# Kernel tuning notes

Hardware: AMD Instinct MI355X
Metric: run time of the kernel (lower is better)

Reference implementation:

```python
import jax, jax.numpy as jnp
import numpy as np

ALPHA = 1000.0


def setup_inputs() -> dict:
    key = jax.random.key(0)
    ks = jax.random.split(key, 5)
    B, D_in, K = 8192, 2048, 256  # K = n_clusters = embed_dim (square cluster_reps)
    x = jax.random.normal(ks[0], (B, D_in), dtype=jnp.float32)
    W_enc = jax.random.normal(ks[1], (D_in, K), dtype=jnp.float32) * (1.0 / np.sqrt(D_in))
    b_enc = jnp.zeros((K,), dtype=jnp.float32)
    W_dec = jax.random.normal(ks[2], (K, D_in), dtype=jnp.float32) * (1.0 / np.sqrt(K))
    b_dec = jnp.zeros((D_in,), dtype=jnp.float32)
    cluster_reps = jax.random.normal(ks[3], (K, K), dtype=jnp.float32)
    return {"x": x, "W_enc": W_enc, "b_enc": b_enc, "W_dec": W_dec,
            "b_dec": b_dec, "cluster_reps": cluster_reps}


def reference(x, W_enc, b_enc, W_dec, b_dec, cluster_reps):
    # Autoencoder (linear MLP stand-in for the injected module)
    emb = x @ W_enc + b_enc                    # [B, K]
    reconstruction = emb @ W_dec + b_dec       # [B, D_in]

    # Squared Euclidean distance to each cluster rep, in GEMM form: [B, K]
    # dist[b, k] = ||emb_b||^2 - 2 emb_b . c_k + ||c_k||^2
    dist = (jnp.sum(emb * emb, axis=1, keepdims=True)
            - 2.0 * (emb @ cluster_reps.T)
            + jnp.sum(cluster_reps * cluster_reps, axis=1)[None, :])

    stack_dist = dist.T                        # [K, B] (matches torch.stack over clusters)
    min_dist = jnp.min(stack_dist, axis=0)     # [B]
    stack_exp = jnp.exp(-ALPHA * (stack_dist - min_dist[None, :]))  # stable softmin
    softmax = stack_exp / jnp.sum(stack_exp, axis=0, keepdims=True)
    weighted_dist = stack_dist * softmax       # [K, B]
    return weighted_dist, reconstruction
```

## Files before the change

kernel.cpp:

```cpp
#include <hip/hip_runtime.h>

#define ALPHA_F 1000.0f

typedef _Float16 half8 __attribute__((ext_vector_type(8)));
typedef float floatx4 __attribute__((ext_vector_type(4)));

__device__ __forceinline__ void gload_lds16(const void* g, void* l) {
    __builtin_amdgcn_global_load_lds(
        (const __attribute__((address_space(1))) unsigned int*)g,
        (__attribute__((address_space(3))) unsigned int*)l, 16, 0, 0);
}

__global__ __launch_bounds__(256) void split_wenc(
    const float* __restrict__ W, _Float16* __restrict__ Wh, _Float16* __restrict__ Wl)
{
    const int q = blockIdx.x * 256 + threadIdx.x;
    const int n = q & 255, k8 = q >> 8;
    const int k = k8 * 8;
    half8 h, l;
    #pragma unroll
    for (int i = 0; i < 8; ++i) {
        const float v = W[(size_t)(k + i) * 256 + n] * 256.0f;
        const _Float16 hi = (_Float16)v;
        h[i] = hi;
        l[i] = (_Float16)(v - (float)hi);
    }
    const int kc = k >> 5, nt = n >> 4;
    const int lane = (n & 15) | ((k8 & 3) << 4);
    const size_t idx = (size_t)((kc * 16 + nt) * 64 + lane) * 8;
    *(half8*)(Wh + idx) = h;
    *(half8*)(Wl + idx) = l;
}

__global__ __launch_bounds__(256) void split_wdec(
    const float* __restrict__ W, _Float16* __restrict__ Wh)
{
    const int q = blockIdx.x * 256 + threadIdx.x;
    const int n = q & 2047, k8 = q >> 11;
    const int k = k8 * 8;
    half8 h;
    #pragma unroll
    for (int i = 0; i < 8; ++i) h[i] = (_Float16)W[(size_t)(k + i) * 2048 + n];
    const int kc = k8 >> 2, nt = n >> 4;
    const int lane = (n & 15) | ((k8 & 3) << 4);
    *(half8*)(Wh + (size_t)((kc * 128 + nt) * 64 + lane) * 8) = h;
}

__global__ __launch_bounds__(256) void split_creps(
    const float* __restrict__ C, _Float16* __restrict__ Ch, _Float16* __restrict__ Cl)
{
    const int q = blockIdx.x * 256 + threadIdx.x;
    const int n = q & 255, j8 = q >> 8;
    const int j = j8 * 8;
    half8 h, l;
    #pragma unroll
    for (int i = 0; i < 8; ++i) {
        const float v = C[(size_t)n * 256 + j + i];
        const _Float16 hi = (_Float16)v;
        h[i] = hi;
        l[i] = (_Float16)((v - (float)hi) * 2048.0f);
    }
    const int jc = j >> 5, nt = n >> 4;
    const int lane = (n & 15) | ((j8 & 3) << 4);
    const size_t idx = (size_t)((jc * 16 + nt) * 64 + lane) * 8;
    *(half8*)(Ch + idx) = h;
    *(half8*)(Cl + idx) = l;
}

__global__ __launch_bounds__(256) void emb_gemm(
    const float* __restrict__ x, const _Float16* __restrict__ Wh,
    const _Float16* __restrict__ Wl, float* __restrict__ P)
{
    __shared__ _Float16 Ah[4 * 64 * 8], Al[4 * 64 * 8];
    __shared__ _Float16 Bh[16 * 64 * 8], Bl[16 * 64 * 8];
    const int t = threadIdx.x, lane = t & 63, w = t >> 6;
    const int kk = blockIdx.x;
    const int mb = blockIdx.y;
    const int m0 = mb * 64;

    const int am = t >> 2, q = t & 3;
    _Float16* AhW = Ah + (((am >> 4) * 64) + ((am & 15) | (q << 4))) * 8;
    _Float16* AlW = Al + (((am >> 4) * 64) + ((am & 15) | (q << 4))) * 8;
    const float* xP = x + (size_t)(m0 + am) * 2048 + kk * 512 + q * 8;

    floatx4 acc[4][4] = {};

    for (int it = 0; it < 16; ++it) {
        const float4 v0 = *(const float4*)(xP + it * 32);
        const float4 v1 = *(const float4*)(xP + it * 32 + 4);
        const int kc = kk * 16 + it;
        __syncthreads();
        const _Float16* bh_src = Wh + (size_t)kc * 16 * 512;
        const _Float16* bl_src = Wl + (size_t)kc * 16 * 512;
        #pragma unroll
        for (int i = 0; i < 4; ++i) {
            const int c = w * 4 + i;
            gload_lds16(bh_src + (size_t)c * 512 + lane * 8, Bh + c * 512);
            gload_lds16(bl_src + (size_t)c * 512 + lane * 8, Bl + c * 512);
        }
        half8 h8, l8;
        {
            const float vv[8] = {v0.x, v0.y, v0.z, v0.w, v1.x, v1.y, v1.z, v1.w};
            #pragma unroll
            for (int i = 0; i < 8; ++i) {
                const _Float16 hi = (_Float16)vv[i];
                h8[i] = hi;
                l8[i] = (_Float16)(vv[i] - (float)hi);
            }
        }
        *(half8*)AhW = h8;
        *(half8*)AlW = l8;
        __syncthreads();

        half8 ah[4], al[4], bh[4], bl[4];
        #pragma unroll
        for (int s = 0; s < 4; ++s) {
            ah[s] = *(const half8*)(Ah + (s * 64 + lane) * 8);
            al[s] = *(const half8*)(Al + (s * 64 + lane) * 8);
        }
        #pragma unroll
        for (int ni = 0; ni < 4; ++ni) {
            bh[ni] = *(const half8*)(Bh + ((w * 4 + ni) * 64 + lane) * 8);
            bl[ni] = *(const half8*)(Bl + ((w * 4 + ni) * 64 + lane) * 8);
        }
        #pragma unroll
        for (int mi = 0; mi < 4; ++mi) {
            #pragma unroll
            for (int ni = 0; ni < 4; ++ni) {
                acc[mi][ni] = __builtin_amdgcn_mfma_f32_16x16x32_f16(ah[mi], bl[ni], acc[mi][ni], 0, 0, 0);
                acc[mi][ni] = __builtin_amdgcn_mfma_f32_16x16x32_f16(al[mi], bh[ni], acc[mi][ni], 0, 0, 0);
                acc[mi][ni] = __builtin_amdgcn_mfma_f32_16x16x32_f16(ah[mi], bh[ni], acc[mi][ni], 0, 0, 0);
            }
        }
    }

    float* Pk = P + (size_t)kk * 2097152;
    #pragma unroll
    for (int mi = 0; mi < 4; ++mi) {
        #pragma unroll
        for (int ni = 0; ni < 4; ++ni) {
            const int col = w * 64 + ni * 16 + (lane & 15);
            const int rowBase = m0 + mi * 16 + (lane >> 4) * 4;
            #pragma unroll
            for (int r = 0; r < 4; ++r)
                Pk[(size_t)(rowBase + r) * 256 + col] = acc[mi][ni][r];
        }
    }
}

__global__ __launch_bounds__(256) void finalize(
    const float* __restrict__ P, const float* __restrict__ b_enc,
    _Float16* __restrict__ eh, _Float16* __restrict__ el,
    float* __restrict__ enorm)
{
    const int t = threadIdx.x;
    const int row = blockIdx.x * 8 + (t >> 5);
    const int q = t & 31;
    const float* p = P + (size_t)row * 256 + q * 8;

    float4 s0 = *(const float4*)(p);
    float4 s1 = *(const float4*)(p + 4);
    #pragma unroll
    for (int kk = 1; kk < 4; ++kk) {
        const float4 a0 = *(const float4*)(p + (size_t)kk * 2097152);
        const float4 a1 = *(const float4*)(p + (size_t)kk * 2097152 + 4);
        s0.x += a0.x; s0.y += a0.y; s0.z += a0.z; s0.w += a0.w;
        s1.x += a1.x; s1.y += a1.y; s1.z += a1.z; s1.w += a1.w;
    }
    const float4 b0 = *(const float4*)(b_enc + q * 8);
    const float4 b1 = *(const float4*)(b_enc + q * 8 + 4);
    const float inv = 1.0f / 256.0f;
    float v[8];
    v[0] = s0.x * inv + b0.x; v[1] = s0.y * inv + b0.y;
    v[2] = s0.z * inv + b0.z; v[3] = s0.w * inv + b0.w;
    v[4] = s1.x * inv + b1.x; v[5] = s1.y * inv + b1.y;
    v[6] = s1.z * inv + b1.z; v[7] = s1.w * inv + b1.w;

    half8 h, l;
    float ssq = 0.0f;
    #pragma unroll
    for (int i = 0; i < 8; ++i) {
        const _Float16 hi = (_Float16)v[i];
        h[i] = hi;
        l[i] = (_Float16)((v[i] - (float)hi) * 2048.0f);
        ssq += v[i] * v[i];
    }
    const size_t idx = (size_t)(((row >> 4) * 8 + (q >> 2)) * 64
                                + ((row & 15) | ((q & 3) << 4))) * 8;
    *(half8*)(eh + idx) = h;
    *(half8*)(el + idx) = l;

    #pragma unroll
    for (int off = 16; off >= 1; off >>= 1) ssq += __shfl_xor(ssq, off, 64);
    if ((t & 31) == 0) enorm[row] = ssq;
}

__global__ __launch_bounds__(256) void recon_gemm(
    const _Float16* __restrict__ embh, const _Float16* __restrict__ Wdh,
    const float* __restrict__ b_dec, float* __restrict__ out)
{
    __shared__ _Float16 Ah[8 * 64 * 8];
    __shared__ _Float16 Bh[8 * 64 * 8];
    const int t = threadIdx.x, lane = t & 63, w = t >> 6;
    const int wm = w >> 1, wn = w & 1;
    const int nb = blockIdx.x, mb = blockIdx.y;

    floatx4 acc[4][4] = {};

    for (int kc = 0; kc < 8; ++kc) {
        __syncthreads();
        #pragma unroll
        for (int i = 0; i < 2; ++i) {
            const int c = w * 2 + i;
            gload_lds16(embh + (size_t)(((mb * 8 + c) * 8 + kc) * 64 + lane) * 8, Ah + c * 512);
            gload_lds16(Wdh + (size_t)((kc * 128 + nb * 8 + c) * 64 + lane) * 8, Bh + c * 512);
        }
        __syncthreads();
        half8 a[4], b[4];
        #pragma unroll
        for (int mi = 0; mi < 4; ++mi) a[mi] = *(const half8*)(Ah + ((wm * 4 + mi) * 64 + lane) * 8);
        #pragma unroll
        for (int ni = 0; ni < 4; ++ni) b[ni] = *(const half8*)(Bh + ((wn * 4 + ni) * 64 + lane) * 8);
        #pragma unroll
        for (int mi = 0; mi < 4; ++mi)
            #pragma unroll
            for (int ni = 0; ni < 4; ++ni)
                acc[mi][ni] = __builtin_amdgcn_mfma_f32_16x16x32_f16(a[mi], b[ni], acc[mi][ni], 0, 0, 0);
    }

    #pragma unroll
    for (int ni = 0; ni < 4; ++ni) {
        const int col = nb * 128 + (wn * 4 + ni) * 16 + (lane & 15);
        const float bias = b_dec[col];
        #pragma unroll
        for (int mi = 0; mi < 4; ++mi) {
            const int rowBase = mb * 128 + (wm * 4 + mi) * 16 + (lane >> 4) * 4;
            #pragma unroll
            for (int r = 0; r < 4; ++r)
                out[(size_t)(rowBase + r) * 2048 + col] = acc[mi][ni][r] + bias;
        }
    }
}

__global__ __launch_bounds__(256) void row_sumsq(
    const float* __restrict__ src, float* __restrict__ dst)
{
    const int wid = threadIdx.x >> 6, lane = threadIdx.x & 63;
    const int row = blockIdx.x * 4 + wid;
    const float4 v = *(const float4*)(src + (size_t)row * 256 + lane * 4);
    float s = v.x * v.x + v.y * v.y + v.z * v.z + v.w * v.w;
    #pragma unroll
    for (int off = 32; off >= 1; off >>= 1) s += __shfl_xor(s, off, 64);
    if (lane == 0) dst[row] = s;
}

__global__ __launch_bounds__(256) void dist_softmin(
    const _Float16* __restrict__ eh, const _Float16* __restrict__ el,
    const _Float16* __restrict__ ch, const _Float16* __restrict__ cl,
    const float* __restrict__ enorm, const float* __restrict__ cnorm,
    float* __restrict__ out)
{
    __shared__ float D[32 * 257];
    __shared__ float MINV[32], SUMV[32];
    const int t = threadIdx.x, lane = t & 63, w = t >> 6;
    const int b0 = blockIdx.x * 32;
    const int mt0 = blockIdx.x * 2;

    floatx4 acc[2][4] = {}, accX[2][4] = {};
    for (int kc = 0; kc < 8; ++kc) {
        half8 ah[2], al[2];
        #pragma unroll
        for (int mi = 0; mi < 2; ++mi) {
            const size_t ab = (size_t)(((mt0 + mi) * 8 + kc) * 64 + lane) * 8;
            ah[mi] = *(const half8*)(eh + ab);
            al[mi] = *(const half8*)(el + ab);
        }
        #pragma unroll
        for (int ni = 0; ni < 4; ++ni) {
            const size_t bb = (size_t)((kc * 16 + (w * 4 + ni)) * 64 + lane) * 8;
            const half8 bh = *(const half8*)(ch + bb);
            const half8 bl = *(const half8*)(cl + bb);
            #pragma unroll
            for (int mi = 0; mi < 2; ++mi) {
                acc[mi][ni]  = __builtin_amdgcn_mfma_f32_16x16x32_f16(ah[mi], bh, acc[mi][ni], 0, 0, 0);
                accX[mi][ni] = __builtin_amdgcn_mfma_f32_16x16x32_f16(ah[mi], bl, accX[mi][ni], 0, 0, 0);
                accX[mi][ni] = __builtin_amdgcn_mfma_f32_16x16x32_f16(al[mi], bh, accX[mi][ni], 0, 0, 0);
            }
        }
    }

    const float invs = 1.0f / 2048.0f;
    #pragma unroll
    for (int mi = 0; mi < 2; ++mi) {
        #pragma unroll
        for (int ni = 0; ni < 4; ++ni) {
            const int k = w * 64 + ni * 16 + (lane & 15);
            const float cn = cnorm[k];
            #pragma unroll
            for (int r = 0; r < 4; ++r) {
                const int rl = mi * 16 + (lane >> 4) * 4 + r;
                const float S = acc[mi][ni][r] + accX[mi][ni][r] * invs;
                D[rl * 257 + k] = enorm[b0 + rl] - 2.0f * S + cn;
            }
        }
    }
    __syncthreads();

    #pragma unroll
    for (int rr = 0; rr < 8; ++rr) {
        const int r = w * 8 + rr;
        const float d0 = D[r * 257 + lane +   0];
        const float d1 = D[r * 257 + lane +  64];
        const float d2 = D[r * 257 + lane + 128];
        const float d3 = D[r * 257 + lane + 192];
        float mn = fminf(fminf(d0, d1), fminf(d2, d3));
        #pragma unroll
        for (int off = 32; off >= 1; off >>= 1) mn = fminf(mn, __shfl_xor(mn, off, 64));
        float s = expf(-ALPHA_F * (d0 - mn)) + expf(-ALPHA_F * (d1 - mn))
                + expf(-ALPHA_F * (d2 - mn)) + expf(-ALPHA_F * (d3 - mn));
        #pragma unroll
        for (int off = 32; off >= 1; off >>= 1) s += __shfl_xor(s, off, 64);
        if (lane == 0) { MINV[r] = mn; SUMV[r] = s; }
    }
    __syncthreads();

    const int b = t & 31, kg = t >> 5;
    const float mn = MINV[b], sv = SUMV[b];
    #pragma unroll
    for (int kk = 0; kk < 32; ++kk) {
        const int k = kk * 8 + kg;
        const float dv = D[b * 257 + k];
        out[(size_t)k * 8192 + b0 + b] = dv * expf(-ALPHA_F * (dv - mn)) / sv;
    }
}

extern "C" void kernel_launch(void* const* d_in, const int* in_sizes, int n_in,
                              void* d_out, int out_size, void* d_ws, size_t ws_size,
                              hipStream_t stream) {
    const float* x     = (const float*)d_in[0];
    const float* W_enc = (const float*)d_in[1];
    const float* b_enc = (const float*)d_in[2];
    const float* W_dec = (const float*)d_in[3];
    const float* b_dec = (const float*)d_in[4];
    const float* creps = (const float*)d_in[5];

    float* out_w   = (float*)d_out;
    float* out_rec = out_w + (size_t)256 * 8192;
    float* P       = out_rec;

    float*     enorm = (float*)d_ws;
    float*     cnorm = enorm + 8192;
    _Float16*  embh  = (_Float16*)(cnorm + 256);
    _Float16*  embl  = embh + (size_t)8192 * 256;
    _Float16*  Whf   = embl + (size_t)8192 * 256;
    _Float16*  Wlf   = Whf + (size_t)2048 * 256;
    _Float16*  Wdh   = Wlf + (size_t)2048 * 256;
    _Float16*  crh   = Wdh + (size_t)256 * 2048;
    _Float16*  crl   = crh + (size_t)256 * 256;

    split_wenc<<<256, 256, 0, stream>>>(W_enc, Whf, Wlf);
    split_wdec<<<256, 256, 0, stream>>>(W_dec, Wdh);
    split_creps<<<32, 256, 0, stream>>>(creps, crh, crl);
    row_sumsq<<<64, 256, 0, stream>>>(creps, cnorm);

    emb_gemm<<<dim3(4, 128), 256, 0, stream>>>(x, Whf, Wlf, P);

    finalize<<<1024, 256, 0, stream>>>(P, b_enc, embh, embl, enorm);

    dist_softmin<<<256, 256, 0, stream>>>(embh, embl, crh, crl, enorm, cnorm, out_w);

    recon_gemm<<<dim3(16, 64), 256, 0, stream>>>(embh, Wdh, b_dec, out_rec);
}
```

Baseline: 210.2 us.

## Double split-K factor for emb_gemm and store partials in fragment layout

The encoder GEMM's split-K factor goes from 4 to 8, doubling the grid to 1024 blocks for better CU occupancy. Partial sums are now written as contiguous floatx4 fragments per thread instead of scattered row-major stores. The finalize kernel reads those fragments, reduces the eight partials, transposes through LDS and then produces the hi/lo fp16 embedding and row norms. This trades twice the partial-sum traffic for more parallelism and coalesced stores.

```diff
diff --git a/kernel.cpp b/kernel.cpp
--- a/kernel.cpp
+++ b/kernel.cpp
@@ -81,14 +81,14 @@
     const int am = t >> 2, q = t & 3;
     _Float16* AhW = Ah + (((am >> 4) * 64) + ((am & 15) | (q << 4))) * 8;
     _Float16* AlW = Al + (((am >> 4) * 64) + ((am & 15) | (q << 4))) * 8;
-    const float* xP = x + (size_t)(m0 + am) * 2048 + kk * 512 + q * 8;
+    const float* xP = x + (size_t)(m0 + am) * 2048 + kk * 256 + q * 8;
 
     floatx4 acc[4][4] = {};
 
-    for (int it = 0; it < 16; ++it) {
+    for (int it = 0; it < 8; ++it) {
         const float4 v0 = *(const float4*)(xP + it * 32);
         const float4 v1 = *(const float4*)(xP + it * 32 + 4);
-        const int kc = kk * 16 + it;
+        const int kc = kk * 8 + it;
         __syncthreads();
         const _Float16* bh_src = Wh + (size_t)kc * 16 * 512;
         const _Float16* bl_src = Wl + (size_t)kc * 16 * 512;
@@ -134,18 +134,12 @@
         }
     }
 
-    float* Pk = P + (size_t)kk * 2097152;
-    #pragma unroll
-    for (int mi = 0; mi < 4; ++mi) {
-        #pragma unroll
-        for (int ni = 0; ni < 4; ++ni) {
-            const int col = w * 64 + ni * 16 + (lane & 15);
-            const int rowBase = m0 + mi * 16 + (lane >> 4) * 4;
-            #pragma unroll
-            for (int r = 0; r < 4; ++r)
-                Pk[(size_t)(rowBase + r) * 256 + col] = acc[mi][ni][r];
-        }
-    }
+    float* Pb = P + ((size_t)(kk * 128 + mb) * 16) * 1024;
+    #pragma unroll
+    for (int mi = 0; mi < 4; ++mi)
+        #pragma unroll
+        for (int ni = 0; ni < 4; ++ni)
+            *(floatx4*)(Pb + (size_t)(mi * 4 + ni) * 1024 + t * 4) = acc[mi][ni];
 }
 
 __global__ __launch_bounds__(256) void finalize(
@@ -153,46 +147,65 @@
     _Float16* __restrict__ eh, _Float16* __restrict__ el,
     float* __restrict__ enorm)
 {
-    const int t = threadIdx.x;
-    const int row = blockIdx.x * 8 + (t >> 5);
-    const int q = t & 31;
-    const float* p = P + (size_t)row * 256 + q * 8;
-
-    float4 s0 = *(const float4*)(p);
-    float4 s1 = *(const float4*)(p + 4);
-    #pragma unroll
-    for (int kk = 1; kk < 4; ++kk) {
-        const float4 a0 = *(const float4*)(p + (size_t)kk * 2097152);
-        const float4 a1 = *(const float4*)(p + (size_t)kk * 2097152 + 4);
-        s0.x += a0.x; s0.y += a0.y; s0.z += a0.z; s0.w += a0.w;
-        s1.x += a1.x; s1.y += a1.y; s1.z += a1.z; s1.w += a1.w;
-    }
-    const float4 b0 = *(const float4*)(b_enc + q * 8);
-    const float4 b1 = *(const float4*)(b_enc + q * 8 + 4);
+    __shared__ float femb[32 * 257];
+    const int t = threadIdx.x, lane = t & 63, w = t >> 6;
+    const int mb = blockIdx.x >> 1, half_ = blockIdx.x & 1;
+    const int mi2 = half_ * 2;
+
+    floatx4 acc[2][4] = {};
+    #pragma unroll
+    for (int kk = 0; kk < 8; ++kk) {
+        const float* Pb = P + ((size_t)(kk * 128 + mb) * 16) * 1024;
+        #pragma unroll
+        for (int dmi = 0; dmi < 2; ++dmi)
+            #pragma unroll
+            for (int ni = 0; ni < 4; ++ni) {
+                const floatx4 v = *(const floatx4*)(Pb + (size_t)((mi2 + dmi) * 4 + ni) * 1024 + t * 4);
+                acc[dmi][ni] += v;
+            }
+    }
+
     const float inv = 1.0f / 256.0f;
-    float v[8];
-    v[0] = s0.x * inv + b0.x; v[1] = s0.y * inv + b0.y;
-    v[2] = s0.z * inv + b0.z; v[3] = s0.w * inv + b0.w;
-    v[4] = s1.x * inv + b1.x; v[5] = s1.y * inv + b1.y;
-    v[6] = s1.z * inv + b1.z; v[7] = s1.w * inv + b1.w;
-
-    half8 h, l;
+    #pragma unroll
+    for (int dmi = 0; dmi < 2; ++dmi) {
+        #pragma unroll
+        for (int ni = 0; ni < 4; ++ni) {
+            const int col = w * 64 + ni * 16 + (lane & 15);
+            const float bias = b_enc[col];
+            const int rowL = dmi * 16 + (lane >> 4) * 4;
+            #pragma unroll
+            for (int r = 0; r < 4; ++r)
+                femb[(rowL + r) * 257 + col] = acc[dmi][ni][r] * inv + bias;
+        }
+    }
+    __syncthreads();
+
+    const int rowL = t >> 3;
     float ssq = 0.0f;
     #pragma unroll
-    for (int i = 0; i < 8; ++i) {
-        const _Float16 hi = (_Float16)v[i];
-        h[i] = hi;
-        l[i] = (_Float16)((v[i] - (float)hi) * 2048.0f);
-        ssq += v[i] * v[i];
-    }
-    const size_t idx = (size_t)(((row >> 4) * 8 + (q >> 2)) * 64
-                                + ((row & 15) | ((q & 3) << 4))) * 8;
-    *(half8*)(eh + idx) = h;
-    *(half8*)(el + idx) = l;
-
-    #pragma unroll
-    for (int off = 16; off >= 1; off >>= 1) ssq += __shfl_xor(ssq, off, 64);
-    if ((t & 31) == 0) enorm[row] = ssq;
+    for (int oo = 0; oo < 4; ++oo) {
+        const int oid = t * 4 + oo;
+        const int q = oid & 31;
+        const float* src = femb + rowL * 257 + q * 8;
+        half8 h, l;
+        #pragma unroll
+        for (int i = 0; i < 8; ++i) {
+            const float v = src[i];
+            const _Float16 hi = (_Float16)v;
+            h[i] = hi;
+            l[i] = (_Float16)((v - (float)hi) * 2048.0f);
+            ssq += v * v;
+        }
+        const int grow = mb * 64 + half_ * 32 + rowL;
+        const size_t idx = (size_t)(((grow >> 4) * 8 + (q >> 2)) * 64
+                                    + ((grow & 15) | ((q & 3) << 4))) * 8;
+        *(half8*)(eh + idx) = h;
+        *(half8*)(el + idx) = l;
+    }
+    ssq += __shfl_xor(ssq, 1, 64);
+    ssq += __shfl_xor(ssq, 2, 64);
+    ssq += __shfl_xor(ssq, 4, 64);
+    if ((t & 7) == 0) enorm[mb * 64 + half_ * 32 + rowL] = ssq;
 }
 
 __global__ __launch_bounds__(256) void recon_gemm(
@@ -363,9 +376,9 @@
     split_creps<<<32, 256, 0, stream>>>(creps, crh, crl);
     row_sumsq<<<64, 256, 0, stream>>>(creps, cnorm);
 
-    emb_gemm<<<dim3(4, 128), 256, 0, stream>>>(x, Whf, Wlf, P);
-
-    finalize<<<1024, 256, 0, stream>>>(P, b_enc, embh, embl, enorm);
+    emb_gemm<<<dim3(8, 128), 256, 0, stream>>>(x, Whf, Wlf, P);
+
+    finalize<<<256, 256, 0, stream>>>(P, b_enc, embh, embl, enorm);
 
     dist_softmin<<<256, 256, 0, stream>>>(embh, embl, crh, crl, enorm, cnorm, out_w);
 
```

Result: slower. 220.2 us (+4.8%).

## Merge weight-prep kernels and fuse split-K finalize into distance/softmin kernel

Applied to the files above, without the earlier changes.

The four small preprocessing kernels are merged into one launch that dispatches on block index. The finalize step, which reduces the split-K partials, adds the bias and computes row norms, now runs inside the distance/softmin kernel. That kernel keeps the fp32 embedding in LDS and builds the fp16 hi/lo split in registers, so the global eh/el/enorm round-trip disappears. This cuts launch count and global traffic. The cost is that the fused kernel runs only 256 blocks for the reduction phase where finalize used 1024, which lowers parallelism when reading the partial sums.

```diff
diff --git a/kernel.cpp b/kernel.cpp
--- a/kernel.cpp
+++ b/kernel.cpp
@@ -11,60 +11,68 @@
         (__attribute__((address_space(3))) unsigned int*)l, 16, 0, 0);
 }
 
-__global__ __launch_bounds__(256) void split_wenc(
-    const float* __restrict__ W, _Float16* __restrict__ Wh, _Float16* __restrict__ Wl)
+__global__ __launch_bounds__(256) void prep(
+    const float* __restrict__ W_enc, const float* __restrict__ W_dec,
+    const float* __restrict__ creps,
+    _Float16* __restrict__ Wh, _Float16* __restrict__ Wl,
+    _Float16* __restrict__ Wdh,
+    _Float16* __restrict__ Ch, _Float16* __restrict__ Cl,
+    float* __restrict__ cnorm)
 {
-    const int q = blockIdx.x * 256 + threadIdx.x;
-    const int n = q & 255, k8 = q >> 8;
-    const int k = k8 * 8;
-    half8 h, l;
-    #pragma unroll
-    for (int i = 0; i < 8; ++i) {
-        const float v = W[(size_t)(k + i) * 256 + n] * 256.0f;
-        const _Float16 hi = (_Float16)v;
-        h[i] = hi;
-        l[i] = (_Float16)(v - (float)hi);
-    }
-    const int kc = k >> 5, nt = n >> 4;
-    const int lane = (n & 15) | ((k8 & 3) << 4);
-    const size_t idx = (size_t)((kc * 16 + nt) * 64 + lane) * 8;
-    *(half8*)(Wh + idx) = h;
-    *(half8*)(Wl + idx) = l;
-}
-
-__global__ __launch_bounds__(256) void split_wdec(
-    const float* __restrict__ W, _Float16* __restrict__ Wh)
-{
-    const int q = blockIdx.x * 256 + threadIdx.x;
-    const int n = q & 2047, k8 = q >> 11;
-    const int k = k8 * 8;
-    half8 h;
-    #pragma unroll
-    for (int i = 0; i < 8; ++i) h[i] = (_Float16)W[(size_t)(k + i) * 2048 + n];
-    const int kc = k8 >> 2, nt = n >> 4;
-    const int lane = (n & 15) | ((k8 & 3) << 4);
-    *(half8*)(Wh + (size_t)((kc * 128 + nt) * 64 + lane) * 8) = h;
-}
-
-__global__ __launch_bounds__(256) void split_creps(
-    const float* __restrict__ C, _Float16* __restrict__ Ch, _Float16* __restrict__ Cl)
-{
-    const int q = blockIdx.x * 256 + threadIdx.x;
-    const int n = q & 255, j8 = q >> 8;
-    const int j = j8 * 8;
-    half8 h, l;
-    #pragma unroll
-    for (int i = 0; i < 8; ++i) {
-        const float v = C[(size_t)n * 256 + j + i];
-        const _Float16 hi = (_Float16)v;
-        h[i] = hi;
-        l[i] = (_Float16)((v - (float)hi) * 2048.0f);
-    }
-    const int jc = j >> 5, nt = n >> 4;
-    const int lane = (n & 15) | ((j8 & 3) << 4);
-    const size_t idx = (size_t)((jc * 16 + nt) * 64 + lane) * 8;
-    *(half8*)(Ch + idx) = h;
-    *(half8*)(Cl + idx) = l;
+    const int bid = blockIdx.x;
+    if (bid < 256) {
+        const int q = bid * 256 + threadIdx.x;
+        const int n = q & 255, k8 = q >> 8;
+        const int k = k8 * 8;
+        half8 h, l;
+        #pragma unroll
+        for (int i = 0; i < 8; ++i) {
+            const float v = W_enc[(size_t)(k + i) * 256 + n] * 256.0f;
+            const _Float16 hi = (_Float16)v;
+            h[i] = hi;
+            l[i] = (_Float16)(v - (float)hi);
+        }
+        const int kc = k >> 5, nt = n >> 4;
+        const int lane = (n & 15) | ((k8 & 3) << 4);
+        const size_t idx = (size_t)((kc * 16 + nt) * 64 + lane) * 8;
+        *(half8*)(Wh + idx) = h;
+        *(half8*)(Wl + idx) = l;
+    } else if (bid < 512) {
+        const int q = (bid - 256) * 256 + threadIdx.x;
+        const int n = q & 2047, k8 = q >> 11;
+        const int k = k8 * 8;
+        half8 h;
+        #pragma unroll
+        for (int i = 0; i < 8; ++i) h[i] = (_Float16)W_dec[(size_t)(k + i) * 2048 + n];
+        const int kc = k8 >> 2, nt = n >> 4;
+        const int lane = (n & 15) | ((k8 & 3) << 4);
+        *(half8*)(Wdh + (size_t)((kc * 128 + nt) * 64 + lane) * 8) = h;
+    } else if (bid < 544) {
+        const int q = (bid - 512) * 256 + threadIdx.x;
+        const int n = q & 255, j8 = q >> 8;
+        const int j = j8 * 8;
+        half8 h, l;
+        #pragma unroll
+        for (int i = 0; i < 8; ++i) {
+            const float v = creps[(size_t)n * 256 + j + i];
+            const _Float16 hi = (_Float16)v;
+            h[i] = hi;
+            l[i] = (_Float16)((v - (float)hi) * 2048.0f);
+        }
+        const int jc = j >> 5, nt = n >> 4;
+        const int lane = (n & 15) | ((j8 & 3) << 4);
+        const size_t idx = (size_t)((jc * 16 + nt) * 64 + lane) * 8;
+        *(half8*)(Ch + idx) = h;
+        *(half8*)(Cl + idx) = l;
+    } else {
+        const int wid = threadIdx.x >> 6, lane = threadIdx.x & 63;
+        const int row = (bid - 544) * 4 + wid;
+        const float4 v = *(const float4*)(creps + (size_t)row * 256 + lane * 4);
+        float s = v.x * v.x + v.y * v.y + v.z * v.z + v.w * v.w;
+        #pragma unroll
+        for (int off = 32; off >= 1; off >>= 1) s += __shfl_xor(s, off, 64);
+        if (lane == 0) cnorm[row] = s;
+    }
 }
 
 __global__ __launch_bounds__(256) void emb_gemm(
@@ -148,51 +156,142 @@
     }
 }
 
-__global__ __launch_bounds__(256) void finalize(
+__global__ __launch_bounds__(256) void fin_dist(
     const float* __restrict__ P, const float* __restrict__ b_enc,
-    _Float16* __restrict__ eh, _Float16* __restrict__ el,
-    float* __restrict__ enorm)
+    const _Float16* __restrict__ ch, const _Float16* __restrict__ cl,
+    const float* __restrict__ cnorm,
+    _Float16* __restrict__ ehg, float* __restrict__ out)
 {
-    const int t = threadIdx.x;
-    const int row = blockIdx.x * 8 + (t >> 5);
-    const int q = t & 31;
-    const float* p = P + (size_t)row * 256 + q * 8;
-
-    float4 s0 = *(const float4*)(p);
-    float4 s1 = *(const float4*)(p + 4);
-    #pragma unroll
-    for (int kk = 1; kk < 4; ++kk) {
-        const float4 a0 = *(const float4*)(p + (size_t)kk * 2097152);
-        const float4 a1 = *(const float4*)(p + (size_t)kk * 2097152 + 4);
-        s0.x += a0.x; s0.y += a0.y; s0.z += a0.z; s0.w += a0.w;
-        s1.x += a1.x; s1.y += a1.y; s1.z += a1.z; s1.w += a1.w;
-    }
-    const float4 b0 = *(const float4*)(b_enc + q * 8);
-    const float4 b1 = *(const float4*)(b_enc + q * 8 + 4);
-    const float inv = 1.0f / 256.0f;
-    float v[8];
-    v[0] = s0.x * inv + b0.x; v[1] = s0.y * inv + b0.y;
-    v[2] = s0.z * inv + b0.z; v[3] = s0.w * inv + b0.w;
-    v[4] = s1.x * inv + b1.x; v[5] = s1.y * inv + b1.y;
-    v[6] = s1.z * inv + b1.z; v[7] = s1.w * inv + b1.w;
-
-    half8 h, l;
-    float ssq = 0.0f;
-    #pragma unroll
-    for (int i = 0; i < 8; ++i) {
-        const _Float16 hi = (_Float16)v[i];
-        h[i] = hi;
-        l[i] = (_Float16)((v[i] - (float)hi) * 2048.0f);
-        ssq += v[i] * v[i];
-    }
-    const size_t idx = (size_t)(((row >> 4) * 8 + (q >> 2)) * 64
-                                + ((row & 15) | ((q & 3) << 4))) * 8;
-    *(half8*)(eh + idx) = h;
-    *(half8*)(el + idx) = l;
-
-    #pragma unroll
-    for (int off = 16; off >= 1; off >>= 1) ssq += __shfl_xor(ssq, off, 64);
-    if ((t & 31) == 0) enorm[row] = ssq;
+    __shared__ float femb[32 * 257];
+    __shared__ float ENORM[32], MINV[32], SUMV[32];
+    const int t = threadIdx.x, lane = t & 63, w = t >> 6;
+    const int b0 = blockIdx.x * 32;
+    const int row = t >> 3, c8 = t & 7;
+
+    {
+        const float* p0 = P + (size_t)(b0 + row) * 256 + c8 * 32;
+        float4 v[8];
+        #pragma unroll
+        for (int i = 0; i < 8; ++i) v[i] = *(const float4*)(p0 + i * 4);
+        #pragma unroll
+        for (int kk = 1; kk < 4; ++kk) {
+            const float* pk = p0 + (size_t)kk * 2097152;
+            #pragma unroll
+            for (int i = 0; i < 8; ++i) {
+                const float4 a = *(const float4*)(pk + i * 4);
+                v[i].x += a.x; v[i].y += a.y; v[i].z += a.z; v[i].w += a.w;
+            }
+        }
+        const float inv = 1.0f / 256.0f;
+        float ssq = 0.0f;
+        #pragma unroll
+        for (int i = 0; i < 8; ++i) {
+            const float4 b = *(const float4*)(b_enc + c8 * 32 + i * 4);
+            float4 e;
+            e.x = v[i].x * inv + b.x; e.y = v[i].y * inv + b.y;
+            e.z = v[i].z * inv + b.z; e.w = v[i].w * inv + b.w;
+            femb[row * 257 + c8 * 32 + i * 4 + 0] = e.x;
+            femb[row * 257 + c8 * 32 + i * 4 + 1] = e.y;
+            femb[row * 257 + c8 * 32 + i * 4 + 2] = e.z;
+            femb[row * 257 + c8 * 32 + i * 4 + 3] = e.w;
+            ssq += e.x * e.x; ssq += e.y * e.y; ssq += e.z * e.z; ssq += e.w * e.w;
+        }
+        ssq += __shfl_xor(ssq, 1, 64);
+        ssq += __shfl_xor(ssq, 2, 64);
+        ssq += __shfl_xor(ssq, 4, 64);
+        if (c8 == 0) ENORM[row] = ssq;
+    }
+    __syncthreads();
+
+    {
+        const int grow = b0 + row;
+        #pragma unroll
+        for (int oo = 0; oo < 4; ++oo) {
+            const int q = c8 * 4 + oo;
+            const float* src = femb + row * 257 + q * 8;
+            half8 h;
+            #pragma unroll
+            for (int i = 0; i < 8; ++i) h[i] = (_Float16)src[i];
+            const size_t idx = (size_t)(((grow >> 4) * 8 + (q >> 2)) * 64
+                                        + ((grow & 15) | ((q & 3) << 4))) * 8;
+            *(half8*)(ehg + idx) = h;
+        }
+    }
+
+    floatx4 acc[2][4] = {}, accX[2][4] = {};
+    const int arow16 = lane & 15, aoct = lane >> 4;
+    for (int kc = 0; kc < 8; ++kc) {
+        half8 ah[2], al[2];
+        #pragma unroll
+        for (int mi = 0; mi < 2; ++mi) {
+            const float* fp = femb + (mi * 16 + arow16) * 257 + kc * 32 + aoct * 8;
+            #pragma unroll
+            for (int j = 0; j < 8; ++j) {
+                const float vv = fp[j];
+                const _Float16 hi = (_Float16)vv;
+                ah[mi][j] = hi;
+                al[mi][j] = (_Float16)((vv - (float)hi) * 2048.0f);
+            }
+        }
+        #pragma unroll
+        for (int ni = 0; ni < 4; ++ni) {
+            const size_t bb = (size_t)((kc * 16 + (w * 4 + ni)) * 64 + lane) * 8;
+            const half8 bh = *(const half8*)(ch + bb);
+            const half8 bl = *(const half8*)(cl + bb);
+            #pragma unroll
+            for (int mi = 0; mi < 2; ++mi) {
+                acc[mi][ni]  = __builtin_amdgcn_mfma_f32_16x16x32_f16(ah[mi], bh, acc[mi][ni], 0, 0, 0);
+                accX[mi][ni] = __builtin_amdgcn_mfma_f32_16x16x32_f16(ah[mi], bl, accX[mi][ni], 0, 0, 0);
+                accX[mi][ni] = __builtin_amdgcn_mfma_f32_16x16x32_f16(al[mi], bh, accX[mi][ni], 0, 0, 0);
+            }
+        }
+    }
+    __syncthreads();
+
+    float* D = femb;
+    const float invs = 1.0f / 2048.0f;
+    #pragma unroll
+    for (int mi = 0; mi < 2; ++mi) {
+        #pragma unroll
+        for (int ni = 0; ni < 4; ++ni) {
+            const int k = w * 64 + ni * 16 + (lane & 15);
+            const float cn = cnorm[k];
+            #pragma unroll
+            for (int r = 0; r < 4; ++r) {
+                const int rl = mi * 16 + (lane >> 4) * 4 + r;
+                const float S = acc[mi][ni][r] + accX[mi][ni][r] * invs;
+                D[rl * 257 + k] = ENORM[rl] - 2.0f * S + cn;
+            }
+        }
+    }
+    __syncthreads();
+
+    #pragma unroll
+    for (int rr = 0; rr < 8; ++rr) {
+        const int r = w * 8 + rr;
+        const float d0 = D[r * 257 + lane +   0];
+        const float d1 = D[r * 257 + lane +  64];
+        const float d2 = D[r * 257 + lane + 128];
+        const float d3 = D[r * 257 + lane + 192];
+        float mn = fminf(fminf(d0, d1), fminf(d2, d3));
+        #pragma unroll
+        for (int off = 32; off >= 1; off >>= 1) mn = fminf(mn, __shfl_xor(mn, off, 64));
+        float s = expf(-ALPHA_F * (d0 - mn)) + expf(-ALPHA_F * (d1 - mn))
+                + expf(-ALPHA_F * (d2 - mn)) + expf(-ALPHA_F * (d3 - mn));
+        #pragma unroll
+        for (int off = 32; off >= 1; off >>= 1) s += __shfl_xor(s, off, 64);
+        if (lane == 0) { MINV[r] = mn; SUMV[r] = s; }
+    }
+    __syncthreads();
+
+    const int b = t & 31, kg = t >> 5;
+    const float mn = MINV[b], sv = SUMV[b];
+    #pragma unroll
+    for (int kk = 0; kk < 32; ++kk) {
+        const int k = kk * 8 + kg;
+        const float dv = D[b * 257 + k];
+        out[(size_t)k * 8192 + b0 + b] = dv * expf(-ALPHA_F * (dv - mn)) / sv;
+    }
 }
 
 __global__ __launch_bounds__(256) void recon_gemm(
@@ -242,98 +341,6 @@
     }
 }
 
-__global__ __launch_bounds__(256) void row_sumsq(
-    const float* __restrict__ src, float* __restrict__ dst)
-{
-    const int wid = threadIdx.x >> 6, lane = threadIdx.x & 63;
-    const int row = blockIdx.x * 4 + wid;
-    const float4 v = *(const float4*)(src + (size_t)row * 256 + lane * 4);
-    float s = v.x * v.x + v.y * v.y + v.z * v.z + v.w * v.w;
-    #pragma unroll
-    for (int off = 32; off >= 1; off >>= 1) s += __shfl_xor(s, off, 64);
-    if (lane == 0) dst[row] = s;
-}
-
-__global__ __launch_bounds__(256) void dist_softmin(
-    const _Float16* __restrict__ eh, const _Float16* __restrict__ el,
-    const _Float16* __restrict__ ch, const _Float16* __restrict__ cl,
-    const float* __restrict__ enorm, const float* __restrict__ cnorm,
-    float* __restrict__ out)
-{
-    __shared__ float D[32 * 257];
-    __shared__ float MINV[32], SUMV[32];
-    const int t = threadIdx.x, lane = t & 63, w = t >> 6;
-    const int b0 = blockIdx.x * 32;
-    const int mt0 = blockIdx.x * 2;
-
-    floatx4 acc[2][4] = {}, accX[2][4] = {};
-    for (int kc = 0; kc < 8; ++kc) {
-        half8 ah[2], al[2];
-        #pragma unroll
-        for (int mi = 0; mi < 2; ++mi) {
-            const size_t ab = (size_t)(((mt0 + mi) * 8 + kc) * 64 + lane) * 8;
-            ah[mi] = *(const half8*)(eh + ab);
-            al[mi] = *(const half8*)(el + ab);
-        }
-        #pragma unroll
-        for (int ni = 0; ni < 4; ++ni) {
-            const size_t bb = (size_t)((kc * 16 + (w * 4 + ni)) * 64 + lane) * 8;
-            const half8 bh = *(const half8*)(ch + bb);
-            const half8 bl = *(const half8*)(cl + bb);
-            #pragma unroll
-            for (int mi = 0; mi < 2; ++mi) {
-                acc[mi][ni]  = __builtin_amdgcn_mfma_f32_16x16x32_f16(ah[mi], bh, acc[mi][ni], 0, 0, 0);
-                accX[mi][ni] = __builtin_amdgcn_mfma_f32_16x16x32_f16(ah[mi], bl, accX[mi][ni], 0, 0, 0);
-                accX[mi][ni] = __builtin_amdgcn_mfma_f32_16x16x32_f16(al[mi], bh, accX[mi][ni], 0, 0, 0);
-            }
-        }
-    }
-
-    const float invs = 1.0f / 2048.0f;
-    #pragma unroll
-    for (int mi = 0; mi < 2; ++mi) {
-        #pragma unroll
-        for (int ni = 0; ni < 4; ++ni) {
-            const int k = w * 64 + ni * 16 + (lane & 15);
-            const float cn = cnorm[k];
-            #pragma unroll
-            for (int r = 0; r < 4; ++r) {
-                const int rl = mi * 16 + (lane >> 4) * 4 + r;
-                const float S = acc[mi][ni][r] + accX[mi][ni][r] * invs;
-                D[rl * 257 + k] = enorm[b0 + rl] - 2.0f * S + cn;
-            }
-        }
-    }
-    __syncthreads();
-
-    #pragma unroll
-    for (int rr = 0; rr < 8; ++rr) {
-        const int r = w * 8 + rr;
-        const float d0 = D[r * 257 + lane +   0];
-        const float d1 = D[r * 257 + lane +  64];
-        const float d2 = D[r * 257 + lane + 128];
-        const float d3 = D[r * 257 + lane + 192];
-        float mn = fminf(fminf(d0, d1), fminf(d2, d3));
-        #pragma unroll
-        for (int off = 32; off >= 1; off >>= 1) mn = fminf(mn, __shfl_xor(mn, off, 64));
-        float s = expf(-ALPHA_F * (d0 - mn)) + expf(-ALPHA_F * (d1 - mn))
-                + expf(-ALPHA_F * (d2 - mn)) + expf(-ALPHA_F * (d3 - mn));
-        #pragma unroll
-        for (int off = 32; off >= 1; off >>= 1) s += __shfl_xor(s, off, 64);
-        if (lane == 0) { MINV[r] = mn; SUMV[r] = s; }
-    }
-    __syncthreads();
-
-    const int b = t & 31, kg = t >> 5;
-    const float mn = MINV[b], sv = SUMV[b];
-    #pragma unroll
-    for (int kk = 0; kk < 32; ++kk) {
-        const int k = kk * 8 + kg;
-        const float dv = D[b * 257 + k];
-        out[(size_t)k * 8192 + b0 + b] = dv * expf(-ALPHA_F * (dv - mn)) / sv;
-    }
-}
-
 extern "C" void kernel_launch(void* const* d_in, const int* in_sizes, int n_in,
                               void* d_out, int out_size, void* d_ws, size_t ws_size,
                               hipStream_t stream) {
@@ -348,26 +355,19 @@
     float* out_rec = out_w + (size_t)256 * 8192;
     float* P       = out_rec;
 
-    float*     enorm = (float*)d_ws;
-    float*     cnorm = enorm + 8192;
+    float*     cnorm = (float*)d_ws;
     _Float16*  embh  = (_Float16*)(cnorm + 256);
-    _Float16*  embl  = embh + (size_t)8192 * 256;
-    _Float16*  Whf   = embl + (size_t)8192 * 256;
+    _Float16*  Whf   = embh + (size_t)8192 * 256;
     _Float16*  Wlf   = Whf + (size_t)2048 * 256;
     _Float16*  Wdh   = Wlf + (size_t)2048 * 256;
     _Float16*  crh   = Wdh + (size_t)256 * 2048;
     _Float16*  crl   = crh + (size_t)256 * 256;
 
-    split_wenc<<<256, 256, 0, stream>>>(W_enc, Whf, Wlf);
-    split_wdec<<<256, 256, 0, stream>>>(W_dec, Wdh);
-    split_creps<<<32, 256, 0, stream>>>(creps, crh, crl);
-    row_sumsq<<<64, 256, 0, stream>>>(creps, cnorm);
+    prep<<<608, 256, 0, stream>>>(W_enc, W_dec, creps, Whf, Wlf, Wdh, crh, crl, cnorm);
 
     emb_gemm<<<dim3(4, 128), 256, 0, stream>>>(x, Whf, Wlf, P);
 
-    finalize<<<1024, 256, 0, stream>>>(P, b_enc, embh, embl, enorm);
-
-    dist_softmin<<<256, 256, 0, stream>>>(embh, embl, crh, crl, enorm, cnorm, out_w);
+    fin_dist<<<256, 256, 0, stream>>>(P, b_enc, crh, crl, cnorm, embh, out_w);
 
     recon_gemm<<<dim3(16, 64), 256, 0, stream>>>(embh, Wdh, b_dec, out_rec);
 }
```

Measured after the change: 204.3 us. -2.8%, faster.
